# Performance work log

Hardware: AMD Instinct MI355X
Metric: run time of the kernel (lower is better)

Reference implementation:

```python
import jax, jax.numpy as jnp
import numpy as np

WINDOW = 256  # attention_window (band half-width w; band is 2w+1 wide)


def _longformer(q, k, v, global_attention_mask, padding_mask, num_global, w):
    B, H, S, D = q.shape
    BH = B * H
    G = int(num_global)
    scale = jnp.sqrt(jnp.asarray(D, q.dtype))
    qf = q.reshape(BH, S, D)
    kf = k.reshape(BH, S, D)
    vf = v.reshape(BH, S, D)
    is_global = jnp.repeat(global_attention_mask.astype(bool), H, axis=0)  # [BH,S]
    pad_ok = jnp.repeat(padding_mask.astype(bool), H, axis=0)              # [BH,S]
    NEG = jnp.asarray(-jnp.inf, q.dtype)

    # ---- banded local qk scores via overlapping 3-chunk trick ----
    nc = S // w
    qc = qf.reshape(BH, nc, w, D)
    kp = jnp.pad(kf, ((0, 0), (w, w), (0, 0))).reshape(BH, nc + 2, w, D)
    k3 = jnp.concatenate([kp[:, :-2], kp[:, 1:-1], kp[:, 2:]], axis=2)     # [BH,nc,3w,D]
    scores3 = jnp.einsum('bcxd,bcyd->bcxy', qc, k3) / scale                # [BH,nc,w,3w]
    band_idx = jnp.arange(w)[:, None] + jnp.arange(2 * w + 1)[None, :]     # [w,2w+1]
    band = jnp.take_along_axis(scores3, band_idx[None, None], axis=3)
    band = band.reshape(BH, S, 2 * w + 1)                                  # score[i,t] = q_i . k_{i-w+t}

    # ---- local-band masking: out-of-bounds, global key columns, padding ----
    rel = jnp.arange(S)[:, None] + jnp.arange(-w, w + 1)[None, :]          # [S,2w+1]
    oob = (rel < 0) | (rel >= S)
    relc = jnp.clip(rel, 0, S - 1)
    glob_key = is_global[:, relc]                                          # [BH,S,2w+1]
    pad_key = pad_ok[:, relc]
    band = jnp.where(oob[None] | glob_key | ~pad_key, NEG, band)

    # ---- all tokens attend to the (sparse) global keys ----
    gpos = jnp.argsort((~is_global).astype(jnp.int32), axis=-1)[:, :G]     # stable: global positions in order
    gk = jnp.take_along_axis(kf, gpos[..., None], axis=1)                  # [BH,G,D]
    gv = jnp.take_along_axis(vf, gpos[..., None], axis=1)
    g_ok = jnp.take_along_axis(pad_ok, gpos, axis=1)                       # [BH,G]
    gscores = jnp.einsum('bsd,bgd->bsg', qf, gk) / scale
    gscores = jnp.where(g_ok[:, None, :], gscores, NEG)

    # ---- joint softmax over [global | local band] ----
    probs = jax.nn.softmax(jnp.concatenate([gscores, band], axis=-1), axis=-1)
    gprobs, lprobs = probs[..., :G], probs[..., G:]

    ctx = jnp.einsum('bsg,bgd->bsd', gprobs, gv)
    vp = jnp.pad(vf, ((0, 0), (w, w), (0, 0))).reshape(BH, nc + 2, w, D)
    v3 = jnp.concatenate([vp[:, :-2], vp[:, 1:-1], vp[:, 2:]], axis=2)     # [BH,nc,3w,D]
    p3 = jnp.zeros((BH, nc, w, 3 * w), probs.dtype)
    p3 = p3.at[:, :, jnp.arange(w)[:, None], band_idx].set(lprobs.reshape(BH, nc, w, 2 * w + 1))
    ctx = ctx + jnp.einsum('bcxy,bcyd->bcxd', p3, v3).reshape(BH, S, D)

    # ---- global tokens attend to every token (full attention rows) ----
    gq = jnp.take_along_axis(qf, gpos[..., None], axis=1)                  # [BH,G,D]
    rscores = jnp.einsum('bgd,bsd->bgs', gq, kf) / scale
    rscores = jnp.where(pad_ok[:, None, :], rscores, NEG)
    rprobs = jax.nn.softmax(rscores, axis=-1)
    vmask = jnp.where(pad_ok[..., None], vf, jnp.asarray(0.0, vf.dtype))
    ctx_g = jnp.einsum('bgs,bsd->bgd', rprobs, vmask)
    ctx = ctx.at[jnp.arange(BH)[:, None], gpos].set(ctx_g)

    return ctx.reshape(B, H, S, D)


def setup_inputs() -> dict:
    key = jax.random.key(0)
    kq, kk, kv = jax.random.split(key, 3)
    B, H, S, D, G = 1, 16, 4096, 64, 64
    q = jax.random.normal(kq, (B, H, S, D), jnp.float32)
    k = jax.random.normal(kk, (B, H, S, D), jnp.float32)
    v = jax.random.normal(kv, (B, H, S, D), jnp.float32)
    global_attention_mask = jnp.zeros((B, S), jnp.int32).at[:, :G].set(1)
    padding_mask = jnp.ones((B, S), jnp.int32)
    return {"q": q, "k": k, "v": v, "global_attention_mask": global_attention_mask,
            "padding_mask": padding_mask, "num_global": G}


def reference(q, k, v, global_attention_mask, padding_mask, num_global):
    return _longformer(q, k, v, global_attention_mask, padding_mask, num_global, WINDOW)
```

## Files before the change

### kernel.cpp

```cpp
#include <hip/hip_runtime.h>
#include <hip/hip_bf16.h>

#define SLEN 4096
#define NH   16
#define DH   64
#define WW   256
#define GMAX 64

typedef unsigned short u16;
typedef unsigned int   u32;
typedef unsigned long long u64;
typedef __attribute__((ext_vector_type(8))) short bf16x8;
typedef __attribute__((ext_vector_type(4))) float f32x4;

#define MFMA16(a,b,c) __builtin_amdgcn_mfma_f32_16x16x32_bf16((a),(b),(c),0,0,0)

static __device__ __forceinline__ int imin(int a, int b) { return a < b ? a : b; }
static __device__ __forceinline__ int imax(int a, int b) { return a > b ? a : b; }

__device__ __forceinline__ u32 cvtpk(float lo, float hi) {
  u32 r;
  asm("v_cvt_pk_bf16_f32 %0, %1, %2" : "=v"(r) : "v"(lo), "v"(hi));
  return r;
}
__device__ __forceinline__ u16 f2bf(float x) {
  u32 u = __float_as_uint(x);
  u32 r = (u + 0x7fffu + ((u >> 16) & 1u)) >> 16;
  return (u16)r;
}

__device__ __forceinline__ void gload16(const u16* src, u16* lds_base) {
  __builtin_amdgcn_global_load_lds((const __attribute__((address_space(1))) u32*)src,
                                   (__attribute__((address_space(3))) u32*)lds_base,
                                   16, 0, 0);
}

__global__ __launch_bounds__(256) void lf_prep1(
    const float* __restrict__ k, const float* __restrict__ v,
    const int* __restrict__ gmask, const int* __restrict__ pmask, const int* __restrict__ nGp,
    u16* __restrict__ kB, u16* __restrict__ vtB,
    int* __restrict__ gpos, unsigned char* __restrict__ gmsk,
    unsigned char* __restrict__ msk, unsigned char* __restrict__ cleanmap) {
  const int bid = blockIdx.x;
  const int tid = threadIdx.x;
  if (bid < 2048) {
    int i = (bid * 256 + tid) * 8;
    float4 v0 = *(const float4*)(k + i);
    float4 v1 = *(const float4*)(k + i + 4);
    uint4 w;
    w.x = cvtpk(v0.x, v0.y);
    w.y = cvtpk(v0.z, v0.w);
    w.z = cvtpk(v1.x, v1.y);
    w.w = cvtpk(v1.z, v1.w);
    *(uint4*)(kB + i) = w;
    return;
  }
  if (bid < 3072) {
    __shared__ float t[64][65];
    int b = bid - 2048;
    int h = b >> 6, s0 = (b & 63) << 6;
    int tile = h * 64 + (b & 63);
    int r = tid >> 2, c0 = (tid & 3) << 4;
    const float* src = v + ((size_t)h * SLEN + s0 + r) * DH + c0;
#pragma unroll
    for (int j = 0; j < 16; j += 4) {
      float4 a = *(const float4*)(src + j);
      t[r][c0 + j]     = a.x;
      t[r][c0 + j + 1] = a.y;
      t[r][c0 + j + 2] = a.z;
      t[r][c0 + j + 3] = a.w;
    }
    __syncthreads();
    int d = tid >> 2, j0 = (tid & 3) << 4;
    int grp  = j0 & 32;
    int half = (j0 & 16) ? 4 : 0;
    u16* dst = vtB + ((size_t)tile * 64 + d) * 64 + grp;
#pragma unroll
    for (int q4 = 0; q4 < 4; ++q4) {
      uint2 val;
      val.x = cvtpk(t[j0 + 4 * q4 + 0][d], t[j0 + 4 * q4 + 1][d]);
      val.y = cvtpk(t[j0 + 4 * q4 + 2][d], t[j0 + 4 * q4 + 3][d]);
      *(uint2*)(dst + 8 * q4 + half) = val;
    }
    return;
  }
  const int G = imin(nGp[0], GMAX);
  for (int s = tid; s < SLEN; s += 256) {
    unsigned char b = (unsigned char)((pmask[s] ? 1 : 0) | (gmask[s] ? 2 : 0));
    msk[s] = b;
  }
  for (int s = SLEN + tid; s < SLEN + 64; s += 256) msk[s] = 0;
  __syncthreads();
  if (tid < 64) {
    int lane = tid;
    if (lane < GMAX) gmsk[lane] = 0;
    int cnt = 0;
    for (int c = 0; c < SLEN / 64 && cnt < G; ++c) {
      int s = c * 64 + lane;
      bool isg = gmask[s] != 0;
      u64 b = __ballot(isg);
      int rank = cnt + (int)__popcll(b & ((1ull << lane) - 1ull));
      if (isg && rank < G) gpos[rank] = s;
      cnt += (int)__popcll(b);
    }
    if (cnt < G) {
      int fill = cnt;
      for (int c = 0; c < SLEN / 64 && fill < G; ++c) {
        int s = c * 64 + lane;
        bool non = gmask[s] == 0;
        u64 b = __ballot(non);
        int rank = fill + (int)__popcll(b & ((1ull << lane) - 1ull));
        if (non && rank < G) gpos[rank] = s;
        fill += (int)__popcll(b);
      }
    }
  }
  __syncthreads();
  if (tid < 64) {
    if (tid < G) {
      int p = gpos[tid];
      gmsk[tid] = (unsigned char)(pmask[p] ? 1 : 0);
      msk[p] = (unsigned char)(msk[p] | 4);
    }
  } else if (tid >= 128) {
    int c = tid - 128;
    if (c < SLEN / 32) {
      unsigned char ok1 = 1, ok2 = 1;
      for (int kk = 0; kk < 32; ++kk) {
        unsigned char b = msk[c * 32 + kk];
        ok1 &= (unsigned char)(((b & 3) == 1) ? 1 : 0);
        ok2 &= (unsigned char)(b & 1);
      }
      cleanmap[c] = (unsigned char)(ok1 | (ok2 << 1));
    }
  }
}

__global__ void lf_gather(const float* __restrict__ qF, const u16* __restrict__ kB,
                          const u16* __restrict__ vtB, const int* __restrict__ gpos,
                          const int* __restrict__ nGp,
                          u16* __restrict__ gq, u16* __restrict__ gk, u16* __restrict__ gvt,
                          float qscale) {
  const int G = imin(nGp[0], GMAX);
  int idx = blockIdx.x * 256 + threadIdx.x;
  int h = idx >> 12, m = (idx >> 6) & 63, d = idx & 63;
  size_t oq = ((size_t)h * GMAX + m) * DH + d;
  int r = m & 31;
  int pos = ((r & 12) << 1) + ((r & 16) >> 2) + (r & 3);
  size_t ot = ((size_t)h * DH + d) * GMAX + (m & 32) + pos;
  if (m < G) {
    int p = gpos[m];
    int pr = p & 31;
    int ppos = ((pr & 12) << 1) + ((pr & 16) >> 2) + (pr & 3);
    gq[oq]  = f2bf(qF[((size_t)h * SLEN + p) * DH + d] * qscale);
    gk[oq]  = kB[((size_t)h * SLEN + p) * DH + d];
    gvt[ot] = vtB[((size_t)(h * 64 + (p >> 6)) * 64 + d) * 64 + (p & 32) + ppos];
  } else {
    gq[oq] = 0; gk[oq] = 0; gvt[ot] = 0;
  }
}

__global__ __launch_bounds__(256) void lf_attn(
    const float* __restrict__ qF, const u16* __restrict__ kB, const u16* __restrict__ vtB,
    const u16* __restrict__ gkB, const u16* __restrict__ gqB, const u16* __restrict__ gvtB,
    const unsigned char* __restrict__ gmskA, const unsigned char* __restrict__ mskA,
    const unsigned char* __restrict__ cleanA, const int* __restrict__ nGp,
    float* __restrict__ out, float* __restrict__ pAcc, float* __restrict__ pL, float qscale) {
  __shared__ __align__(16) u16 sK[2][4096];
  __shared__ __align__(16) u16 sV[2][4096];
  __shared__ u32 sMsk[192];
  __shared__ u32 sGm[16];

  const int tid  = threadIdx.x;
  const int wv   = tid >> 6;
  const int lane = tid & 63;
  const int ql   = lane & 15;
  const int g    = lane >> 4;
  const float NEGV = -1e30f;
  const float MEXP = 24.0f;
  const int G = imin(nGp[0], GMAX);

  const int wg = ((int)blockIdx.x & 7) * 144 + ((int)blockIdx.x >> 3);
  const bool glob = (wg % 9) == 0;

  int off[4][2];
#pragma unroll
  for (int t = 0; t < 4; ++t)
#pragma unroll
    for (int c = 0; c < 2; ++c) {
      int row = 16 * t + ql;
      off[t][c] = (row * 8 + ((c * 4 + g) ^ (row & 7))) * 8;
    }

  f32x4 acc[4];
#pragma unroll
  for (int i = 0; i < 4; ++i) acc[i] = (f32x4){0.f, 0.f, 0.f, 0.f};
  f32x4 lsv = (f32x4){0.f, 0.f, 0.f, 0.f};
  bf16x8 qf0, qf1;

  int h, s0w = 0, sq = 0, t0, nMain, qg = 0, splitIdx = 0;
  int lo_w = 0, hi_w = 0;
  bool hasG = false;
  const u16 *gks = nullptr, *gvs = nullptr;

  if (!glob) {
    int lid = wg - wg / 9 - 1;
    h = lid >> 6;
    int qblk = lid & 63;
    int s0 = qblk << 6;
    s0w = s0 + 16 * wv; sq = s0w + ql;
    t0 = imax(0, qblk - 4);
    int t1 = imin(63, qblk + 4);
    nMain = t1 - t0 + 1;
    hasG = (G > 0);
    lo_w = imax(t0, (s0w - WW) >> 6);
    hi_w = imin(t1, (s0w + 15 + WW) >> 6);
    const float* qr = qF + ((size_t)h * SLEN + sq) * DH;
    float4 a0 = *(const float4*)(qr + 8 * g);
    float4 a1 = *(const float4*)(qr + 8 * g + 4);
    float4 b0 = *(const float4*)(qr + 32 + 8 * g);
    float4 b1 = *(const float4*)(qr + 32 + 8 * g + 4);
    union { u32 w[4]; bf16x8 v; } uq;
    uq.w[0] = cvtpk(a0.x * qscale, a0.y * qscale);
    uq.w[1] = cvtpk(a0.z * qscale, a0.w * qscale);
    uq.w[2] = cvtpk(a1.x * qscale, a1.y * qscale);
    uq.w[3] = cvtpk(a1.z * qscale, a1.w * qscale);
    qf0 = uq.v;
    uq.w[0] = cvtpk(b0.x * qscale, b0.y * qscale);
    uq.w[1] = cvtpk(b0.z * qscale, b0.w * qscale);
    uq.w[2] = cvtpk(b1.x * qscale, b1.y * qscale);
    uq.w[3] = cvtpk(b1.z * qscale, b1.w * qscale);
    qf1 = uq.v;
    gks = gkB + (size_t)h * GMAX * DH;
    gvs = gvtB + (size_t)h * 4096;
  } else {
    int gb = wg / 9;
    h = gb >> 3; splitIdx = gb & 7;
    qg = wv * 16 + ql;
    t0 = splitIdx * 8; nMain = 8;
    const u16* qRow = gqB + ((size_t)h * GMAX + qg) * DH;
    qf0 = *(const bf16x8*)(qRow + 8 * g);
    qf1 = *(const bf16x8*)(qRow + 32 + 8 * g);
  }
  const u16* kbase = kB  + (size_t)h * 64 * 4096;
  const u16* vbase = vtB + (size_t)h * 64 * 4096;
  const int totPh = nMain + (hasG ? 1 : 0);

  const unsigned char cmask = glob ? 2 : 1;
  unsigned char cbyte = 0;
  if (lane < nMain) {
    cbyte = (unsigned char)(cleanA[2 * (t0 + lane)] & cleanA[2 * (t0 + lane) + 1]);
  }
  const u64 cbits = __ballot((cbyte & cmask) != 0);

  auto stage = [&](int p, int b) {
    const u16 *ks, *vs;
    if (hasG && p == 0) { ks = gks; vs = gvs; }
    else {
      int tv = t0 + p - (hasG ? 1 : 0);
      ks = kbase + (size_t)tv * 4096;
      vs = vbase + (size_t)tv * 4096;
    }
#pragma unroll
    for (int j = 0; j < 2; ++j) {
      int gran = (wv * 2 + j) * 64 + lane;
      int sg = gran ^ ((gran >> 3) & 7);
      gload16(ks + (size_t)sg * 8, &sK[b][(wv * 2 + j) * 512]);
      gload16(vs + (size_t)sg * 8, &sV[b][(wv * 2 + j) * 512]);
    }
  };

  auto compute = [&](int p, int buf) {
    const bool isg = (hasG && p == 0);
    const int idx = p - (hasG ? 1 : 0);
    const int tv = t0 + idx;
    const int kb = tv * 64;
    bool doC = glob ? true : (isg || (tv >= lo_w && tv <= hi_w));
    if (!doC) return;
    const u16* sk = &sK[buf][0];
    const u16* sv = &sV[buf][0];
    f32x4 sc[4];
#pragma unroll
    for (int t = 0; t < 4; ++t) sc[t] = (f32x4){0.f, 0.f, 0.f, 0.f};
#pragma unroll
    for (int t = 0; t < 4; ++t) {
      bf16x8 a0 = *(const bf16x8*)(sk + off[t][0]);
      bf16x8 a1 = *(const bf16x8*)(sk + off[t][1]);
      sc[t] = MFMA16(a0, qf0, sc[t]);
      sc[t] = MFMA16(a1, qf1, sc[t]);
    }
    f32x4 pv[4];
    if (isg) {
#pragma unroll
      for (int t = 0; t < 4; ++t) {
        u32 mw = sGm[4 * t + g];
#pragma unroll
        for (int i = 0; i < 4; ++i) {
          float s = ((mw >> (8 * i)) & 1) ? sc[t][i] : NEGV;
          pv[t][i] = __builtin_amdgcn_exp2f(s - MEXP);
        }
      }
    } else {
      bool cl = ((cbits >> idx) & 1) != 0;
      if (!glob) cl = cl && (kb >= s0w + 15 - WW) && (kb + 63 <= s0w + WW);
      if (cl) {
#pragma unroll
        for (int t = 0; t < 4; ++t)
#pragma unroll
          for (int i = 0; i < 4; ++i)
            pv[t][i] = __builtin_amdgcn_exp2f(sc[t][i] - MEXP);
      } else if (glob) {
#pragma unroll
        for (int t = 0; t < 4; ++t) {
          u32 mw = sMsk[(idx << 4) + 4 * t + g];
#pragma unroll
          for (int i = 0; i < 4; ++i) {
            float s = ((mw >> (8 * i)) & 1) ? sc[t][i] : NEGV;
            pv[t][i] = __builtin_amdgcn_exp2f(s - MEXP);
          }
        }
      } else {
#pragma unroll
        for (int t = 0; t < 4; ++t) {
          u32 mw = sMsk[(idx << 4) + 4 * t + g];
#pragma unroll
          for (int i = 0; i < 4; ++i) {
            int kkey = kb + 16 * t + 4 * g + i;
            bool vok = (((mw >> (8 * i)) & 3) == 1) && (kkey >= sq - WW) && (kkey <= sq + WW);
            float s = vok ? sc[t][i] : NEGV;
            pv[t][i] = __builtin_amdgcn_exp2f(s - MEXP);
          }
        }
      }
    }
    lsv += pv[0] + pv[1] + pv[2] + pv[3];
#pragma unroll
    for (int s2 = 0; s2 < 2; ++s2) {
      union { u32 w[4]; bf16x8 v8; } u;
      u.w[0] = cvtpk(pv[2 * s2][0], pv[2 * s2][1]);
      u.w[1] = cvtpk(pv[2 * s2][2], pv[2 * s2][3]);
      u.w[2] = cvtpk(pv[2 * s2 + 1][0], pv[2 * s2 + 1][1]);
      u.w[3] = cvtpk(pv[2 * s2 + 1][2], pv[2 * s2 + 1][3]);
#pragma unroll
      for (int dt = 0; dt < 4; ++dt) {
        bf16x8 vf = *(const bf16x8*)(sv + off[dt][s2]);
        acc[dt] = MFMA16(vf, u.v8, acc[dt]);
      }
    }
  };

  stage(0, 0);
  {
    int nb = nMain << 4;
    if (tid < nb) sMsk[tid] = *(const u32*)(mskA + (t0 << 6) + (tid << 2));
    if (hasG && tid >= 192 && tid < 208) sGm[tid - 192] = *(const u32*)(gmskA + ((tid - 192) << 2));
  }
  __syncthreads();

  for (int p = 0; p < totPh; ++p) {
    if (p + 1 < totPh) {
      stage(p + 1, (p + 1) & 1);
      asm volatile("s_waitcnt vmcnt(4)" ::: "memory");
    } else {
      asm volatile("s_waitcnt vmcnt(0)" ::: "memory");
    }
    __builtin_amdgcn_s_barrier();
    __builtin_amdgcn_sched_barrier(0);
    compute(p, p & 1);
    __builtin_amdgcn_s_barrier();
  }

  float lsum = lsv[0] + lsv[1] + lsv[2] + lsv[3];
  lsum += __shfl_xor(lsum, 16);
  lsum += __shfl_xor(lsum, 32);

  if (!glob) {
    float inv = 1.f / lsum;
    bool skip = (mskA[sq] & 4) != 0;
    if (!skip) {
      float* orow = out + ((size_t)h * SLEN + sq) * DH;
#pragma unroll
      for (int dt = 0; dt < 4; ++dt) {
        f32x4 o = acc[dt] * inv;
        *(f32x4*)(orow + dt * 16 + 4 * g) = o;
      }
    }
  } else {
    float* pa = pAcc + ((size_t)(h * 8 + splitIdx) * 64 + qg) * 64;
#pragma unroll
    for (int dt = 0; dt < 4; ++dt)
      *(f32x4*)&pa[dt * 16 + 4 * g] = acc[dt];
    if (g == 0) pL[(h * 8 + splitIdx) * 64 + qg] = lsum;
  }
}

__global__ void lf_gmerge(const float* __restrict__ pAcc, const float* __restrict__ pL,
                          const int* __restrict__ gpos, const int* __restrict__ nGp,
                          float* __restrict__ out) {
  const int G = imin(nGp[0], GMAX);
  int h = blockIdx.x;
  int tid = threadIdx.x;
#pragma unroll
  for (int it = 0; it < 4; ++it) {
    int v = tid + it * 256;
    int q = v >> 4, d4 = (v & 15) << 2;
    if (q >= G) continue;
    float L = 0.f;
    f32x4 a = (f32x4){0.f, 0.f, 0.f, 0.f};
#pragma unroll
    for (int s = 0; s < 8; ++s) {
      L += pL[(h * 8 + s) * 64 + q];
      a += *(const f32x4*)&pAcc[((size_t)(h * 8 + s) * 64 + q) * 64 + d4];
    }
    *(f32x4*)&out[((size_t)h * SLEN + gpos[q]) * DH + d4] = a * (1.f / L);
  }
}

extern "C" void kernel_launch(void* const* d_in, const int* in_sizes, int n_in,
                              void* d_out, int out_size, void* d_ws, size_t ws_size,
                              hipStream_t stream) {
  const float* q = (const float*)d_in[0];
  const float* k = (const float*)d_in[1];
  const float* v = (const float*)d_in[2];
  const int* gmask = (const int*)d_in[3];
  const int* pmask = (const int*)d_in[4];
  const int* nGp = (const int*)d_in[5];
  float* out = (float*)d_out;
  char* ws = (char*)d_ws;

  constexpr size_t NEL = (size_t)NH * SLEN * DH;
  constexpr size_t OFF_KBF  = 0;
  constexpr size_t OFF_VTBF = OFF_KBF + NEL * 2;
  constexpr size_t OFF_GK   = OFF_VTBF + NEL * 2 + 256;
  constexpr size_t OFF_GQ   = OFF_GK + (size_t)NH * GMAX * DH * 2;
  constexpr size_t OFF_GVT  = OFF_GQ + (size_t)NH * GMAX * DH * 2;
  constexpr size_t OFF_GPOS = OFF_GVT + (size_t)NH * DH * GMAX * 2;
  constexpr size_t OFF_GMSK = OFF_GPOS + 256;
  constexpr size_t OFF_MSK  = OFF_GMSK + 64;
  constexpr size_t OFF_CLEAN = OFF_MSK + SLEN + 64;
  constexpr size_t OFF_PACC = OFF_CLEAN + 256;
  constexpr size_t OFF_PL   = OFF_PACC + (size_t)NH * 8 * 64 * 64 * 4;

  u16* kB  = (u16*)(ws + OFF_KBF);
  u16* vtB = (u16*)(ws + OFF_VTBF);
  u16* gk  = (u16*)(ws + OFF_GK);
  u16* gq  = (u16*)(ws + OFF_GQ);
  u16* gvt = (u16*)(ws + OFF_GVT);
  int* gpos = (int*)(ws + OFF_GPOS);
  unsigned char* gmsk = (unsigned char*)(ws + OFF_GMSK);
  unsigned char* msk  = (unsigned char*)(ws + OFF_MSK);
  unsigned char* clean = (unsigned char*)(ws + OFF_CLEAN);
  float* pAcc = (float*)(ws + OFF_PACC);
  float* pL   = (float*)(ws + OFF_PL);

  const float qscale = 0.125f * 1.4426950408889634f;

  lf_prep1<<<3073, 256, 0, stream>>>(k, v, gmask, pmask, nGp,
                                     kB, vtB, gpos, gmsk, msk, clean);
  lf_gather<<<256, 256, 0, stream>>>(q, kB, vtB, gpos, nGp, gq, gk, gvt, qscale);
  lf_attn<<<1152, 256, 0, stream>>>(q, kB, vtB, gk, gq, gvt, gmsk, msk, clean,
                                    nGp, out, pAcc, pL, qscale);
  lf_gmerge<<<NH, 256, 0, stream>>>(pAcc, pL, gpos, nGp, out);
}
```

Baseline: 53.37 us.

## Process 32 query rows per wave to reuse each staged K/V tile

Each wave now computes two 16-row query tiles against every K/V tile loaded into shared memory. That doubles the query block per workgroup to 128 rows and halves the grid from 1152 to 576 blocks. Global-query blocks are reorganised so that wave pairs split the key tiles by parity, with 16 tiles per block. The aim is to cut the redundant global-to-LDS staging of overlapping band tiles, which should lower memory traffic per query. In exchange, register pressure rises from the doubled accumulators, and the smaller grid may underfill the 256 CUs.

```diff
diff --git a/kernel.cpp b/kernel.cpp
--- a/kernel.cpp
+++ b/kernel.cpp
@@ -168,7 +168,7 @@
     float* __restrict__ out, float* __restrict__ pAcc, float* __restrict__ pL, float qscale) {
   __shared__ __align__(16) u16 sK[2][4096];
   __shared__ __align__(16) u16 sV[2][4096];
-  __shared__ u32 sMsk[192];
+  __shared__ u32 sMsk[256];
   __shared__ u32 sGm[16];
 
   const int tid  = threadIdx.x;
@@ -180,7 +180,7 @@
   const float MEXP = 24.0f;
   const int G = imin(nGp[0], GMAX);
 
-  const int wg = ((int)blockIdx.x & 7) * 144 + ((int)blockIdx.x >> 3);
+  const int wg = ((int)blockIdx.x & 7) * 72 + ((int)blockIdx.x >> 3);
   const bool glob = (wg % 9) == 0;
 
   int off[4][2];
@@ -192,30 +192,22 @@
       off[t][c] = (row * 8 + ((c * 4 + g) ^ (row & 7))) * 8;
     }
 
-  f32x4 acc[4];
-#pragma unroll
-  for (int i = 0; i < 4; ++i) acc[i] = (f32x4){0.f, 0.f, 0.f, 0.f};
-  f32x4 lsv = (f32x4){0.f, 0.f, 0.f, 0.f};
-  bf16x8 qf0, qf1;
-
-  int h, s0w = 0, sq = 0, t0, nMain, qg = 0, splitIdx = 0;
+  f32x4 accA[4], accB[4];
+#pragma unroll
+  for (int i = 0; i < 4; ++i) {
+    accA[i] = (f32x4){0.f, 0.f, 0.f, 0.f};
+    accB[i] = (f32x4){0.f, 0.f, 0.f, 0.f};
+  }
+  f32x4 lsvA = (f32x4){0.f, 0.f, 0.f, 0.f};
+  f32x4 lsvB = (f32x4){0.f, 0.f, 0.f, 0.f};
+  bf16x8 qf0a, qf1a, qf0b, qf1b;
+
+  int h, s0w = 0, t0, nMain, splitIdx = 0, rh = 0, par = 0;
   int lo_w = 0, hi_w = 0;
   bool hasG = false;
   const u16 *gks = nullptr, *gvs = nullptr;
 
-  if (!glob) {
-    int lid = wg - wg / 9 - 1;
-    h = lid >> 6;
-    int qblk = lid & 63;
-    int s0 = qblk << 6;
-    s0w = s0 + 16 * wv; sq = s0w + ql;
-    t0 = imax(0, qblk - 4);
-    int t1 = imin(63, qblk + 4);
-    nMain = t1 - t0 + 1;
-    hasG = (G > 0);
-    lo_w = imax(t0, (s0w - WW) >> 6);
-    hi_w = imin(t1, (s0w + 15 + WW) >> 6);
-    const float* qr = qF + ((size_t)h * SLEN + sq) * DH;
+  auto loadQf32 = [&](const float* qr, bf16x8& f0, bf16x8& f1) {
     float4 a0 = *(const float4*)(qr + 8 * g);
     float4 a1 = *(const float4*)(qr + 8 * g + 4);
     float4 b0 = *(const float4*)(qr + 32 + 8 * g);
@@ -225,22 +217,41 @@
     uq.w[1] = cvtpk(a0.z * qscale, a0.w * qscale);
     uq.w[2] = cvtpk(a1.x * qscale, a1.y * qscale);
     uq.w[3] = cvtpk(a1.z * qscale, a1.w * qscale);
-    qf0 = uq.v;
+    f0 = uq.v;
     uq.w[0] = cvtpk(b0.x * qscale, b0.y * qscale);
     uq.w[1] = cvtpk(b0.z * qscale, b0.w * qscale);
     uq.w[2] = cvtpk(b1.x * qscale, b1.y * qscale);
     uq.w[3] = cvtpk(b1.z * qscale, b1.w * qscale);
-    qf1 = uq.v;
+    f1 = uq.v;
+  };
+
+  if (!glob) {
+    int lid = wg - wg / 9 - 1;
+    h = lid >> 5;
+    int qblk = lid & 31;
+    int s0 = qblk << 7;
+    s0w = s0 + 32 * wv;
+    t0 = imax(0, 2 * qblk - 4);
+    int t1 = imin(63, 2 * qblk + 5);
+    nMain = t1 - t0 + 1;
+    hasG = (G > 0);
+    lo_w = imax(t0, (s0w - WW) >> 6);
+    hi_w = imin(t1, (s0w + 31 + WW) >> 6);
+    loadQf32(qF + ((size_t)h * SLEN + s0w + ql) * DH, qf0a, qf1a);
+    loadQf32(qF + ((size_t)h * SLEN + s0w + 16 + ql) * DH, qf0b, qf1b);
     gks = gkB + (size_t)h * GMAX * DH;
     gvs = gvtB + (size_t)h * 4096;
   } else {
     int gb = wg / 9;
-    h = gb >> 3; splitIdx = gb & 7;
-    qg = wv * 16 + ql;
-    t0 = splitIdx * 8; nMain = 8;
-    const u16* qRow = gqB + ((size_t)h * GMAX + qg) * DH;
-    qf0 = *(const bf16x8*)(qRow + 8 * g);
-    qf1 = *(const bf16x8*)(qRow + 32 + 8 * g);
+    h = gb >> 2; splitIdx = gb & 3;
+    rh = wv >> 1; par = wv & 1;
+    t0 = splitIdx * 16; nMain = 16;
+    const u16* qr0 = gqB + ((size_t)h * GMAX + rh * 32 + ql) * DH;
+    const u16* qr1 = gqB + ((size_t)h * GMAX + rh * 32 + 16 + ql) * DH;
+    qf0a = *(const bf16x8*)(qr0 + 8 * g);
+    qf1a = *(const bf16x8*)(qr0 + 32 + 8 * g);
+    qf0b = *(const bf16x8*)(qr1 + 8 * g);
+    qf1b = *(const bf16x8*)(qr1 + 32 + 8 * g);
   }
   const u16* kbase = kB  + (size_t)h * 64 * 4096;
   const u16* vbase = vtB + (size_t)h * 64 * 4096;
@@ -248,9 +259,8 @@
 
   const unsigned char cmask = glob ? 2 : 1;
   unsigned char cbyte = 0;
-  if (lane < nMain) {
+  if (lane < nMain)
     cbyte = (unsigned char)(cleanA[2 * (t0 + lane)] & cleanA[2 * (t0 + lane) + 1]);
-  }
   const u64 cbits = __ballot((cbyte & cmask) != 0);
 
   auto stage = [&](int p, int b) {
@@ -270,25 +280,8 @@
     }
   };
 
-  auto compute = [&](int p, int buf) {
-    const bool isg = (hasG && p == 0);
-    const int idx = p - (hasG ? 1 : 0);
-    const int tv = t0 + idx;
-    const int kb = tv * 64;
-    bool doC = glob ? true : (isg || (tv >= lo_w && tv <= hi_w));
-    if (!doC) return;
-    const u16* sk = &sK[buf][0];
-    const u16* sv = &sV[buf][0];
-    f32x4 sc[4];
-#pragma unroll
-    for (int t = 0; t < 4; ++t) sc[t] = (f32x4){0.f, 0.f, 0.f, 0.f};
-#pragma unroll
-    for (int t = 0; t < 4; ++t) {
-      bf16x8 a0 = *(const bf16x8*)(sk + off[t][0]);
-      bf16x8 a1 = *(const bf16x8*)(sk + off[t][1]);
-      sc[t] = MFMA16(a0, qf0, sc[t]);
-      sc[t] = MFMA16(a1, qf1, sc[t]);
-    }
+  auto softmax_half = [&](const f32x4 (&sc)[4], int hb, int idx, int kb, bool isg,
+                          bf16x8 (&pf)[2], f32x4& ls) {
     f32x4 pv[4];
     if (isg) {
 #pragma unroll
@@ -302,7 +295,7 @@
       }
     } else {
       bool cl = ((cbits >> idx) & 1) != 0;
-      if (!glob) cl = cl && (kb >= s0w + 15 - WW) && (kb + 63 <= s0w + WW);
+      if (!glob) cl = cl && (kb >= hb + 15 - WW) && (kb + 63 <= hb + WW);
       if (cl) {
 #pragma unroll
         for (int t = 0; t < 4; ++t)
@@ -320,20 +313,21 @@
           }
         }
       } else {
+        int sqq = hb + ql;
 #pragma unroll
         for (int t = 0; t < 4; ++t) {
           u32 mw = sMsk[(idx << 4) + 4 * t + g];
 #pragma unroll
           for (int i = 0; i < 4; ++i) {
             int kkey = kb + 16 * t + 4 * g + i;
-            bool vok = (((mw >> (8 * i)) & 3) == 1) && (kkey >= sq - WW) && (kkey <= sq + WW);
+            bool vok = (((mw >> (8 * i)) & 3) == 1) && (kkey >= sqq - WW) && (kkey <= sqq + WW);
             float s = vok ? sc[t][i] : NEGV;
             pv[t][i] = __builtin_amdgcn_exp2f(s - MEXP);
           }
         }
       }
     }
-    lsv += pv[0] + pv[1] + pv[2] + pv[3];
+    ls += pv[0] + pv[1] + pv[2] + pv[3];
 #pragma unroll
     for (int s2 = 0; s2 < 2; ++s2) {
       union { u32 w[4]; bf16x8 v8; } u;
@@ -341,20 +335,53 @@
       u.w[1] = cvtpk(pv[2 * s2][2], pv[2 * s2][3]);
       u.w[2] = cvtpk(pv[2 * s2 + 1][0], pv[2 * s2 + 1][1]);
       u.w[3] = cvtpk(pv[2 * s2 + 1][2], pv[2 * s2 + 1][3]);
+      pf[s2] = u.v8;
+    }
+  };
+
+  auto compute = [&](int p, int buf) {
+    const bool isg = (hasG && p == 0);
+    const int idx = p - (hasG ? 1 : 0);
+    const int tv = t0 + idx;
+    const int kb = tv * 64;
+    bool doC = glob ? ((idx & 1) == par) : (isg || (tv >= lo_w && tv <= hi_w));
+    if (!doC) return;
+    const u16* sk = &sK[buf][0];
+    const u16* sv = &sV[buf][0];
+    f32x4 scA[4], scB[4];
+#pragma unroll
+    for (int t = 0; t < 4; ++t) {
+      scA[t] = (f32x4){0.f, 0.f, 0.f, 0.f};
+      scB[t] = (f32x4){0.f, 0.f, 0.f, 0.f};
+    }
+#pragma unroll
+    for (int t = 0; t < 4; ++t) {
+      bf16x8 a0 = *(const bf16x8*)(sk + off[t][0]);
+      bf16x8 a1 = *(const bf16x8*)(sk + off[t][1]);
+      scA[t] = MFMA16(a0, qf0a, scA[t]);
+      scA[t] = MFMA16(a1, qf1a, scA[t]);
+      scB[t] = MFMA16(a0, qf0b, scB[t]);
+      scB[t] = MFMA16(a1, qf1b, scB[t]);
+    }
+    bf16x8 pfA[2], pfB[2];
+    softmax_half(scA, s0w, idx, kb, isg, pfA, lsvA);
+    softmax_half(scB, s0w + 16, idx, kb, isg, pfB, lsvB);
+#pragma unroll
+    for (int s2 = 0; s2 < 2; ++s2) {
 #pragma unroll
       for (int dt = 0; dt < 4; ++dt) {
         bf16x8 vf = *(const bf16x8*)(sv + off[dt][s2]);
-        acc[dt] = MFMA16(vf, u.v8, acc[dt]);
+        accA[dt] = MFMA16(vf, pfA[s2], accA[dt]);
+        accB[dt] = MFMA16(vf, pfB[s2], accB[dt]);
       }
     }
   };
 
   stage(0, 0);
-  {
-    int nb = nMain << 4;
-    if (tid < nb) sMsk[tid] = *(const u32*)(mskA + (t0 << 6) + (tid << 2));
-    if (hasG && tid >= 192 && tid < 208) sGm[tid - 192] = *(const u32*)(gmskA + ((tid - 192) << 2));
-  }
+  if (tid < (nMain << 4))
+    sMsk[tid] = *(const u32*)(mskA + (t0 << 6) + (tid << 2));
+  if (hasG && tid >= 208 && tid < 224)
+    sGm[tid - 208] = *(const u32*)(gmskA + ((tid - 208) << 2));
   __syncthreads();
 
   for (int p = 0; p < totPh; ++p) {
@@ -370,27 +397,42 @@
     __builtin_amdgcn_s_barrier();
   }
 
-  float lsum = lsv[0] + lsv[1] + lsv[2] + lsv[3];
-  lsum += __shfl_xor(lsum, 16);
-  lsum += __shfl_xor(lsum, 32);
+  float lsA = lsvA[0] + lsvA[1] + lsvA[2] + lsvA[3];
+  lsA += __shfl_xor(lsA, 16);
+  lsA += __shfl_xor(lsA, 32);
+  float lsB = lsvB[0] + lsvB[1] + lsvB[2] + lsvB[3];
+  lsB += __shfl_xor(lsB, 16);
+  lsB += __shfl_xor(lsB, 32);
 
   if (!glob) {
-    float inv = 1.f / lsum;
-    bool skip = (mskA[sq] & 4) != 0;
-    if (!skip) {
-      float* orow = out + ((size_t)h * SLEN + sq) * DH;
-#pragma unroll
-      for (int dt = 0; dt < 4; ++dt) {
-        f32x4 o = acc[dt] * inv;
-        *(f32x4*)(orow + dt * 16 + 4 * g) = o;
-      }
+    int sqA = s0w + ql, sqB = s0w + 16 + ql;
+    float invA = 1.f / lsA, invB = 1.f / lsB;
+    if (!(mskA[sqA] & 4)) {
+      float* orow = out + ((size_t)h * SLEN + sqA) * DH;
+#pragma unroll
+      for (int dt = 0; dt < 4; ++dt)
+        *(f32x4*)(orow + dt * 16 + 4 * g) = accA[dt] * invA;
+    }
+    if (!(mskA[sqB] & 4)) {
+      float* orow = out + ((size_t)h * SLEN + sqB) * DH;
+#pragma unroll
+      for (int dt = 0; dt < 4; ++dt)
+        *(f32x4*)(orow + dt * 16 + 4 * g) = accB[dt] * invB;
     }
   } else {
-    float* pa = pAcc + ((size_t)(h * 8 + splitIdx) * 64 + qg) * 64;
-#pragma unroll
-    for (int dt = 0; dt < 4; ++dt)
-      *(f32x4*)&pa[dt * 16 + 4 * g] = acc[dt];
-    if (g == 0) pL[(h * 8 + splitIdx) * 64 + qg] = lsum;
+    int s = splitIdx * 2 + par;
+    int qgA = rh * 32 + ql, qgB = rh * 32 + 16 + ql;
+    float* paA = pAcc + ((size_t)(h * 8 + s) * 64 + qgA) * 64;
+    float* paB = pAcc + ((size_t)(h * 8 + s) * 64 + qgB) * 64;
+#pragma unroll
+    for (int dt = 0; dt < 4; ++dt) {
+      *(f32x4*)&paA[dt * 16 + 4 * g] = accA[dt];
+      *(f32x4*)&paB[dt * 16 + 4 * g] = accB[dt];
+    }
+    if (g == 0) {
+      pL[(h * 8 + s) * 64 + qgA] = lsA;
+      pL[(h * 8 + s) * 64 + qgB] = lsB;
+    }
   }
 }
 
@@ -458,7 +500,7 @@
   lf_prep1<<<3073, 256, 0, stream>>>(k, v, gmask, pmask, nGp,
                                      kB, vtB, gpos, gmsk, msk, clean);
   lf_gather<<<256, 256, 0, stream>>>(q, kB, vtB, gpos, nGp, gq, gk, gvt, qscale);
-  lf_attn<<<1152, 256, 0, stream>>>(q, kB, vtB, gk, gq, gvt, gmsk, msk, clean,
-                                    nGp, out, pAcc, pL, qscale);
+  lf_attn<<<576, 256, 0, stream>>>(q, kB, vtB, gk, gq, gvt, gmsk, msk, clean,
+                                   nGp, out, pAcc, pL, qscale);
   lf_gmerge<<<NH, 256, 0, stream>>>(pAcc, pL, gpos, nGp, out);
 }
```

After: 68.33 us. 28.0% more time.
